# Performance work log

Measured on AMD Instinct MI355X. Metric: run time of the kernel, lower is better.

Reference implementation:

```python
import jax, jax.numpy as jnp
import numpy as np

EMBED_DIM = 1024
NUM_HEADS = 16
HEAD_DIM = EMBED_DIM // NUM_HEADS


def setup_inputs() -> dict:
    key = jax.random.key(0)
    ks = jax.random.split(key, 11)
    B, S, D = 4, 2048, EMBED_DIM
    s = 1.0 / np.sqrt(D)
    return {
        "query": jax.random.normal(ks[0], (B, S, D), jnp.float32),
        "key": jax.random.normal(ks[1], (B, S, D), jnp.float32),
        "value": jax.random.normal(ks[2], (B, S, D), jnp.float32),
        "Wq": jax.random.normal(ks[3], (D, D), jnp.float32) * s,
        "bq": jnp.zeros((D,), jnp.float32),
        "Wk": jax.random.normal(ks[4], (D, D), jnp.float32) * s,
        "bk": jnp.zeros((D,), jnp.float32),
        "Wv": jax.random.normal(ks[5], (D, D), jnp.float32) * s,
        "bv": jnp.zeros((D,), jnp.float32),
        "Wo": jax.random.normal(ks[6], (D, D), jnp.float32) * s,
        "bo": jnp.zeros((D,), jnp.float32),
    }


def _split_heads(x):
    B, S, D = x.shape
    return x.reshape(B, S, NUM_HEADS, HEAD_DIM).transpose(0, 2, 1, 3)  # (B,H,S,hd)


def reference(query, key, value, Wq, bq, Wk, bk, Wv, bv, Wo, bo):
    q = _split_heads(query @ Wq + bq)
    k = _split_heads(key @ Wk + bk)
    v = _split_heads(value @ Wv + bv)
    # naive scaled dot-product attention: full (B,H,S,S) scores materialized
    scores = jnp.einsum("bhqd,bhkd->bhqk", q, k) / np.sqrt(HEAD_DIM).astype(np.float32)
    attn = jax.nn.softmax(scores, axis=-1)
    ctx = jnp.einsum("bhqk,bhkd->bhqd", attn, v)
    B, H, S, hd = ctx.shape
    ctx = ctx.transpose(0, 2, 1, 3).reshape(B, S, H * hd)
    return ctx @ Wo + bo
```

## Files before the change

### kernel.cpp

```cpp
#include <hip/hip_runtime.h>

typedef unsigned short u16;
typedef unsigned int u32;
typedef _Float16 f16;
typedef __attribute__((ext_vector_type(8))) _Float16 f16x8;
typedef __attribute__((ext_vector_type(4))) float f32x4;
typedef __attribute__((ext_vector_type(4))) u32 u32x4;
typedef __attribute__((ext_vector_type(2))) u32 u32x2;
typedef __attribute__((ext_vector_type(4))) u16 u16x4;

static __device__ __forceinline__ u16 f16r(float f) {
  return __builtin_bit_cast(u16, (_Float16)f);
}
static __device__ __forceinline__ u32 packh(float a, float b) {
  return __builtin_bit_cast(u32, __builtin_amdgcn_cvt_pkrtz(a, b));
}
static __device__ __forceinline__ void gload16(const u16* g, u16* l) {
  __builtin_amdgcn_global_load_lds((const __attribute__((address_space(1))) void*)g,
                                   (__attribute__((address_space(3))) void*)l, 16, 0, 0);
}
static __device__ __forceinline__ void gload16f(const float* g, float* l) {
  __builtin_amdgcn_global_load_lds((const __attribute__((address_space(1))) void*)g,
                                   (__attribute__((address_space(3))) void*)l, 16, 0, 0);
}

__global__ __launch_bounds__(256) void wtrans4_k(
    const float* __restrict__ Wq, const float* __restrict__ Wk,
    const float* __restrict__ Wv, const float* __restrict__ Wo,
    u16* __restrict__ Tq, u16* __restrict__ Tk, u16* __restrict__ Tv, u16* __restrict__ To) {
  int z = blockIdx.z;
  const float* W = z == 0 ? Wq : z == 1 ? Wk : z == 2 ? Wv : Wo;
  u16* WT = z == 0 ? Tq : z == 1 ? Tk : z == 2 ? Tv : To;
  __shared__ float tile[32][33];
  int k0 = blockIdx.x * 32, n0 = blockIdx.y * 32;
  int t = threadIdx.x;
  int r = t >> 3, c = (t & 7) * 4;
  f32x4 v = *(const f32x4*)&W[(size_t)(k0 + r) * 1024 + n0 + c];
  tile[r][c + 0] = v[0]; tile[r][c + 1] = v[1]; tile[r][c + 2] = v[2]; tile[r][c + 3] = v[3];
  __syncthreads();
  int n = n0 + (t >> 3), kbase = k0 + (t & 7) * 4;
  u16x4 o;
#pragma unroll
  for (int j = 0; j < 4; j++) o[j] = f16r(tile[(t & 7) * 4 + j][t >> 3]);
  int nt = n >> 7, row = n & 127;
  int kt = kbase >> 5, lc = (kbase >> 3) & 3, e = kbase & 7;
  int pc = lc ^ ((row >> 1) & 3);
  *(u16x4*)&WT[((size_t)(nt * 32 + kt) * 128 + row) * 32 + pc * 8 + e] = o;
}

__global__ __launch_bounds__(256) void gemm_qkv_k(
    const float* __restrict__ Aq, const float* __restrict__ Ak, const float* __restrict__ Av,
    const u16* __restrict__ Tq, const u16* __restrict__ Tk, const u16* __restrict__ Tv,
    const float* __restrict__ bq, const float* __restrict__ bk, const float* __restrict__ bv,
    u16* __restrict__ Qo, u16* __restrict__ Ko, u16* __restrict__ Vo, float qscale) {
  int z = blockIdx.z;
  const float* A = z == 0 ? Aq : z == 1 ? Ak : Av;
  const u16* BT = z == 0 ? Tq : z == 1 ? Tk : Tv;
  const float* bias = z == 0 ? bq : z == 1 ? bk : bv;
  u16* out = z == 0 ? Qo : z == 1 ? Ko : Vo;
  int vmode = (z == 2);
  float scale = z == 0 ? qscale : 1.0f;

  __shared__ float As[2][128 * 32];
  __shared__ u16 Bs[2][128 * 32];
  int lid = blockIdx.x;
  int xcd = lid & 7, idx = lid >> 3;
  int bx = idx & 7, by = xcd * 8 + (idx >> 3);
  int n0 = bx * 128, m0 = by * 128;
  int tid = threadIdx.x, lane = tid & 63;
  int w = tid >> 6, wr = w >> 1, wc = w & 1;
  int fq = lane & 15, fc = lane >> 4;
  f32x4 acc[4][4] = {};
  const u16* BTb = BT + (size_t)bx * 131072;

  auto stage = [&](int ks, int sel) {
    const float* Ab = A + (size_t)m0 * 1024 + ks * 32;
#pragma unroll
    for (int i = 0; i < 4; i++) {
      int u = (w * 4 + i) * 64 + lane;
      int row = u >> 3, pc = u & 7;
      int koff = (pc ^ (row & 7)) << 2;
      gload16f(Ab + (size_t)row * 1024 + koff, &As[sel][(w * 4 + i) * 256]);
    }
    const u16* Bt = BTb + ks * 4096;
#pragma unroll
    for (int i = 0; i < 2; i++)
      gload16(Bt + (w * 2 + i) * 512 + lane * 8, &Bs[sel][(w * 2 + i) * 512]);
  };

  stage(0, 0);
  stage(1, 1);
  for (int ks = 0; ks < 32; ks++) {
    int cur = ks & 1;
    if (ks < 31) asm volatile("s_waitcnt vmcnt(6)" ::: "memory");
    else         asm volatile("s_waitcnt vmcnt(0)" ::: "memory");
    __builtin_amdgcn_s_barrier();
    __builtin_amdgcn_sched_barrier(0);
    f16x8 af[4], bfv[4];
#pragma unroll
    for (int mi = 0; mi < 4; mi++) {
      int row = wr * 64 + mi * 16 + fq;
      int pc0 = (2 * fc) ^ (row & 7);
      f32x4 x0 = *(const f32x4*)&As[cur][row * 32 + pc0 * 4];
      f32x4 x1 = *(const f32x4*)&As[cur][row * 32 + (pc0 ^ 1) * 4];
      u32x4 pk = {packh(x0[0], x0[1]), packh(x0[2], x0[3]),
                  packh(x1[0], x1[1]), packh(x1[2], x1[3])};
      af[mi] = __builtin_bit_cast(f16x8, pk);
    }
#pragma unroll
    for (int ni = 0; ni < 4; ni++) {
      int row = wc * 64 + ni * 16 + fq;
      bfv[ni] = *(const f16x8*)&Bs[cur][row * 32 + (fc ^ ((row >> 1) & 3)) * 8];
    }
    __builtin_amdgcn_s_setprio(1);
#pragma unroll
    for (int mi = 0; mi < 4; mi++)
#pragma unroll
      for (int ni = 0; ni < 4; ni++)
        acc[mi][ni] = __builtin_amdgcn_mfma_f32_16x16x32_f16(af[mi], bfv[ni], acc[mi][ni], 0, 0, 0);
    __builtin_amdgcn_s_setprio(0);
    __builtin_amdgcn_sched_barrier(0);
    __builtin_amdgcn_s_barrier();
    if (ks < 30) stage(ks + 2, cur);
  }
#pragma unroll
  for (int mi = 0; mi < 4; mi++)
#pragma unroll
    for (int ni = 0; ni < 4; ni++) {
      int n = n0 + wc * 64 + ni * 16 + fq;
      float bs = bias[n];
      int h = n >> 6, d = n & 63;
#pragma unroll
      for (int r = 0; r < 4; r++) {
        int m = m0 + wr * 64 + mi * 16 + fc * 4 + r;
        int b = m >> 11, s = m & 2047;
        float v = (acc[mi][ni][r] + bs) * scale;
        size_t o;
        if (vmode == 0) {
          int t = s >> 4, fqo = s & 15, kco = d >> 5, fco = (d & 31) >> 3, e = d & 7;
          o = (size_t)(b * 16 + h) * 131072 + (size_t)((((t * 2 + kco) * 64) + fco * 16 + fqo) * 8 + e);
        } else {
          int kvc = s >> 5, dt = d >> 4, fqo = d & 15, fco = (s & 31) >> 3, e = s & 7;
          o = (size_t)(b * 16 + h) * 131072 + (size_t)((((kvc * 4 + dt) * 64) + fco * 16 + fqo) * 8 + e);
        }
        out[o] = f16r(v);
      }
    }
}

__global__ __launch_bounds__(256) void gemm_o_k(
    const u16* __restrict__ Ag, const u16* __restrict__ Bg,
    const float* __restrict__ bias, float* __restrict__ out) {
  __shared__ u16 SA[2][8192];
  __shared__ u16 SB[2][8192];
  int lid = blockIdx.x;
  int xcd = lid & 7, idx = lid >> 3;
  int bx = idx & 7, by = xcd * 8 + (idx >> 3);
  int n0 = bx * 128, m0 = by * 128;
  int tid = threadIdx.x, lane = tid & 63;
  int w = tid >> 6, wr = w >> 1, wc = w & 1;
  int fq = lane & 15, fc = lane >> 4;
  f32x4 acc[4][4] = {};

  auto stage = [&](int ks, int sel) {
    size_t at = ((size_t)by * 16 + ks) * 8192;
    size_t bt = ((size_t)bx * 32 + ks * 2) * 4096;
#pragma unroll
    for (int i = 0; i < 4; i++) {
      int ub = (w * 4 + i) * 512;
      gload16(Ag + at + ub + lane * 8, &SA[sel][ub]);
      gload16(Bg + bt + ub + lane * 8, &SB[sel][ub]);
    }
  };

  stage(0, 0);
  stage(1, 1);
  for (int ks = 0; ks < 16; ks++) {
    int cur = ks & 1;
    if (ks < 15) asm volatile("s_waitcnt vmcnt(8)" ::: "memory");
    else         asm volatile("s_waitcnt vmcnt(0)" ::: "memory");
    __builtin_amdgcn_s_barrier();
    __builtin_amdgcn_sched_barrier(0);
#pragma unroll
    for (int kc = 0; kc < 2; kc++) {
      f16x8 ah[4], bh[4];
#pragma unroll
      for (int mi = 0; mi < 4; mi++) {
        int row = wr * 64 + mi * 16 + fq;
        ah[mi] = *(const f16x8*)&SA[cur][row * 64 + (((kc * 4 + fc) ^ (row & 7)) << 3)];
      }
#pragma unroll
      for (int ni = 0; ni < 4; ni++) {
        int row = wc * 64 + ni * 16 + fq;
        bh[ni] = *(const f16x8*)&SB[cur][kc * 4096 + row * 32 + (fc ^ ((row >> 1) & 3)) * 8];
      }
      __builtin_amdgcn_s_setprio(1);
#pragma unroll
      for (int mi = 0; mi < 4; mi++)
#pragma unroll
        for (int ni = 0; ni < 4; ni++)
          acc[mi][ni] = __builtin_amdgcn_mfma_f32_16x16x32_f16(ah[mi], bh[ni], acc[mi][ni], 0, 0, 0);
      __builtin_amdgcn_s_setprio(0);
    }
    __builtin_amdgcn_sched_barrier(0);
    __builtin_amdgcn_s_barrier();
    if (ks < 14) stage(ks + 2, cur);
  }
#pragma unroll
  for (int mi = 0; mi < 4; mi++)
#pragma unroll
    for (int ni = 0; ni < 4; ni++) {
      int n = n0 + wc * 64 + ni * 16 + fq;
      float bs = bias[n];
#pragma unroll
      for (int r = 0; r < 4; r++) {
        int m = m0 + wr * 64 + mi * 16 + fc * 4 + r;
        out[(size_t)m * 1024 + n] = acc[mi][ni][r] + bs;
      }
    }
}

__global__ __launch_bounds__(512) void attn_k(
    const u16* __restrict__ Q, const u16* __restrict__ Kg, const u16* __restrict__ Vg,
    u16* __restrict__ ctx) {
  int lid = blockIdx.x;
  int bh = (lid & 7) * 8 + (lid >> 6);
  int qb = (lid >> 3) & 7;
  int tid = threadIdx.x, lane = tid & 63, w = tid >> 6;
  const u16* Qf = Q + (size_t)bh * 131072;
  const u16* Kf = Kg + (size_t)bh * 131072;
  const u16* Vf = Vg + (size_t)bh * 131072;
  int fq = lane & 15, fc = lane >> 4;
  int le = lane * 8;
  int q0 = qb * 256 + w * 32;

  __shared__ u16 KL[2][4096];
  __shared__ u16 VL[2][4096];
  __shared__ u16 P[8][1024];

  f16x8 qf[2][2];
#pragma unroll
  for (int mi = 0; mi < 2; mi++)
#pragma unroll
    for (int kc = 0; kc < 2; kc++)
      qf[mi][kc] = *(const f16x8*)&Qf[((((q0 + 16 * mi) >> 4) * 2 + kc) << 9) + le];

  const f16x8 vones = {(_Float16)1.f, (_Float16)1.f, (_Float16)1.f, (_Float16)1.f,
                       (_Float16)1.f, (_Float16)1.f, (_Float16)1.f, (_Float16)1.f};
  f32x4 O[2][4] = {};
  f32x4 Ol[2] = {};

  int pslot = (fc & 1) * 4;
  int pbase = fq + ((fc >> 1) << 4);

  auto stage = [&](int tt, int bb) {
    int qo = (w & 3) * 1024;
    if (w < 4) {
      const u16* Kt = Kf + tt * 4096;
      gload16(Kt + qo + le, &KL[bb][qo]);
      gload16(Kt + qo + 512 + le, &KL[bb][qo + 512]);
    } else {
      const u16* Vt = Vf + tt * 4096;
      gload16(Vt + qo + le, &VL[bb][qo]);
      gload16(Vt + qo + 512 + le, &VL[bb][qo + 512]);
    }
  };

  stage(0, 0);
  stage(1, 1);
  for (int t = 0; t < 32; t++) {
    int buf = t & 1;
    if (t < 31) asm volatile("s_waitcnt vmcnt(2)" ::: "memory");
    else        asm volatile("s_waitcnt vmcnt(0)" ::: "memory");
    __builtin_amdgcn_s_barrier();
    __builtin_amdgcn_sched_barrier(0);

    f16x8 kf[8];
#pragma unroll
    for (int c = 0; c < 8; c++) kf[c] = *(const f16x8*)&KL[buf][c * 512 + le];

    f32x4 sc[2][4] = {};
    __builtin_amdgcn_s_setprio(1);
#pragma unroll
    for (int mi = 0; mi < 2; mi++)
#pragma unroll
      for (int sub = 0; sub < 4; sub++)
#pragma unroll
        for (int kc = 0; kc < 2; kc++)
          sc[mi][sub] = __builtin_amdgcn_mfma_f32_16x16x32_f16(kf[sub * 2 + kc], qf[mi][kc],
                                                               sc[mi][sub], 0, 0, 0);
    __builtin_amdgcn_s_setprio(0);

    f16x8 vf[8];
#pragma unroll
    for (int c = 0; c < 8; c++) vf[c] = *(const f16x8*)&VL[buf][c * 512 + le];

#pragma unroll
    for (int mi = 0; mi < 2; mi++) {
#pragma unroll
      for (int sub = 0; sub < 4; sub++) {
        float p0 = __builtin_amdgcn_exp2f(sc[mi][sub][0]);
        float p1 = __builtin_amdgcn_exp2f(sc[mi][sub][1]);
        float p2 = __builtin_amdgcn_exp2f(sc[mi][sub][2]);
        float p3 = __builtin_amdgcn_exp2f(sc[mi][sub][3]);
        u32x2 pw = {packh(p0, p1), packh(p2, p3)};
        int lp = (pbase + (sub << 5)) & 63;
        *(u32x2*)&P[w][(sub >> 1) * 512 + lp * 8 + pslot] = pw;
      }
      __builtin_amdgcn_s_setprio(1);
#pragma unroll
      for (int ch = 0; ch < 2; ch++) {
        f16x8 pa = *(const f16x8*)&P[w][ch * 512 + lane * 8];
        Ol[mi] = __builtin_amdgcn_mfma_f32_16x16x32_f16(pa, vones, Ol[mi], 0, 0, 0);
#pragma unroll
        for (int db = 0; db < 4; db++)
          O[mi][db] = __builtin_amdgcn_mfma_f32_16x16x32_f16(pa, vf[ch * 4 + db], O[mi][db], 0, 0, 0);
      }
      __builtin_amdgcn_s_setprio(0);
    }

    __builtin_amdgcn_sched_barrier(0);
    __builtin_amdgcn_s_barrier();
    if (t < 30) stage(t + 2, buf);
  }

  int b = bh >> 4, h = bh & 15;
#pragma unroll
  for (int mi = 0; mi < 2; mi++) {
    float linv[4];
#pragma unroll
    for (int r = 0; r < 4; r++) linv[r] = 1.0f / Ol[mi][r];
#pragma unroll
    for (int db = 0; db < 4; db++)
#pragma unroll
      for (int r = 0; r < 4; r++) {
        float v = O[mi][db][r] * linv[r];
        int s = q0 + mi * 16 + fc * 4 + r;
        int mrow = s & 127, mt = b * 16 + (s >> 7);
        int lc = (db * 16 + fq) >> 3, e = fq & 7;
        int pc = lc ^ (mrow & 7);
        size_t o = ((size_t)(mt * 16 + h) * 128 + mrow) * 64 + pc * 8 + e;
        ctx[o] = f16r(v);
      }
  }
}

extern "C" void kernel_launch(void* const* d_in, const int* in_sizes, int n_in,
                              void* d_out, int out_size, void* d_ws, size_t ws_size,
                              hipStream_t stream) {
  const float* query = (const float*)d_in[0];
  const float* key   = (const float*)d_in[1];
  const float* value = (const float*)d_in[2];
  const float* Wq = (const float*)d_in[3];
  const float* bq = (const float*)d_in[4];
  const float* Wk = (const float*)d_in[5];
  const float* bk = (const float*)d_in[6];
  const float* Wv = (const float*)d_in[7];
  const float* bv = (const float*)d_in[8];
  const float* Wo = (const float*)d_in[9];
  const float* bo = (const float*)d_in[10];
  float* out = (float*)d_out;

  char* ws = (char*)d_ws;
  size_t off = 0;
  auto alloc = [&](size_t bytes) {
    char* p = ws + off;
    off += (bytes + 255) & ~(size_t)255;
    return p;
  };
  u16* WqT = (u16*)alloc(1048576 * 2);
  u16* WkT = (u16*)alloc(1048576 * 2);
  u16* WvT = (u16*)alloc(1048576 * 2);
  u16* WoT = (u16*)alloc(1048576 * 2);
  u16* Qbf = (u16*)alloc((size_t)8388608 * 2);
  u16* Kbf = (u16*)alloc((size_t)8388608 * 2);
  u16* ctx = (u16*)alloc((size_t)8388608 * 2);
  u16* Vfb = (u16*)d_out;

  const float QSCALE = 0.125f * 1.44269504f;

  wtrans4_k<<<dim3(32, 32, 4), 256, 0, stream>>>(Wq, Wk, Wv, Wo, WqT, WkT, WvT, WoT);
  gemm_qkv_k<<<dim3(512, 1, 3), 256, 0, stream>>>(query, key, value, WqT, WkT, WvT,
                                                  bq, bk, bv, Qbf, Kbf, Vfb, QSCALE);
  attn_k<<<512, 512, 0, stream>>>(Qbf, Kbf, Vfb, ctx);
  gemm_o_k<<<512, 256, 0, stream>>>(ctx, WoT, bo, out);
}
```

Baseline: 186.2 us.

## Stage QKV GEMM A tiles through registers and store them to LDS as fp16

The QKV projection GEMM now loads the fp32 activation tile into registers, two stages ahead, and converts it to fp16. It writes the packed values into a swizzled fp16 LDS buffer instead of DMA-ing fp32 straight into LDS and converting after every LDS read. This halves A-tile LDS footprint and read traffic and removes the repeated per-wave conversion on reads. The cost is more VGPRs for the prefetch registers, an extra LDS write with an lgkmcnt wait each step, and vmcnt counting that must now cover the register loads too.

```diff
diff --git a/kernel.cpp b/kernel.cpp
--- a/kernel.cpp
+++ b/kernel.cpp
@@ -16,10 +16,6 @@
   return __builtin_bit_cast(u32, __builtin_amdgcn_cvt_pkrtz(a, b));
 }
 static __device__ __forceinline__ void gload16(const u16* g, u16* l) {
-  __builtin_amdgcn_global_load_lds((const __attribute__((address_space(1))) void*)g,
-                                   (__attribute__((address_space(3))) void*)l, 16, 0, 0);
-}
-static __device__ __forceinline__ void gload16f(const float* g, float* l) {
   __builtin_amdgcn_global_load_lds((const __attribute__((address_space(1))) void*)g,
                                    (__attribute__((address_space(3))) void*)l, 16, 0, 0);
 }
@@ -61,8 +57,8 @@
   int vmode = (z == 2);
   float scale = z == 0 ? qscale : 1.0f;
 
-  __shared__ float As[2][128 * 32];
-  __shared__ u16 Bs[2][128 * 32];
+  __shared__ u16 As[2][4096];
+  __shared__ u16 Bs[2][4096];
   int lid = blockIdx.x;
   int xcd = lid & 7, idx = lid >> 3;
   int bx = idx & 7, by = xcd * 8 + (idx >> 3);
@@ -72,57 +68,73 @@
   int fq = lane & 15, fc = lane >> 4;
   f32x4 acc[4][4] = {};
   const u16* BTb = BT + (size_t)bx * 131072;
-
-  auto stage = [&](int ks, int sel) {
-    const float* Ab = A + (size_t)m0 * 1024 + ks * 32;
-#pragma unroll
-    for (int i = 0; i < 4; i++) {
-      int u = (w * 4 + i) * 64 + lane;
-      int row = u >> 3, pc = u & 7;
-      int koff = (pc ^ (row & 7)) << 2;
-      gload16f(Ab + (size_t)row * 1024 + koff, &As[sel][(w * 4 + i) * 256]);
-    }
-    const u16* Bt = BTb + ks * 4096;
-#pragma unroll
-    for (int i = 0; i < 2; i++)
-      gload16(Bt + (w * 2 + i) * 512 + lane * 8, &Bs[sel][(w * 2 + i) * 512]);
-  };
-
-  stage(0, 0);
-  stage(1, 1);
-  for (int ks = 0; ks < 32; ks++) {
-    int cur = ks & 1;
-    if (ks < 31) asm volatile("s_waitcnt vmcnt(6)" ::: "memory");
-    else         asm volatile("s_waitcnt vmcnt(0)" ::: "memory");
-    __builtin_amdgcn_s_barrier();
-    __builtin_amdgcn_sched_barrier(0);
-    f16x8 af[4], bfv[4];
-#pragma unroll
-    for (int mi = 0; mi < 4; mi++) {
-      int row = wr * 64 + mi * 16 + fq;
-      int pc0 = (2 * fc) ^ (row & 7);
-      f32x4 x0 = *(const f32x4*)&As[cur][row * 32 + pc0 * 4];
-      f32x4 x1 = *(const f32x4*)&As[cur][row * 32 + (pc0 ^ 1) * 4];
-      u32x4 pk = {packh(x0[0], x0[1]), packh(x0[2], x0[3]),
-                  packh(x1[0], x1[1]), packh(x1[2], x1[3])};
-      af[mi] = __builtin_bit_cast(f16x8, pk);
-    }
-#pragma unroll
-    for (int ni = 0; ni < 4; ni++) {
-      int row = wc * 64 + ni * 16 + fq;
-      bfv[ni] = *(const f16x8*)&Bs[cur][row * 32 + (fc ^ ((row >> 1) & 3)) * 8];
-    }
-    __builtin_amdgcn_s_setprio(1);
-#pragma unroll
-    for (int mi = 0; mi < 4; mi++)
-#pragma unroll
-      for (int ni = 0; ni < 4; ni++)
-        acc[mi][ni] = __builtin_amdgcn_mfma_f32_16x16x32_f16(af[mi], bfv[ni], acc[mi][ni], 0, 0, 0);
-    __builtin_amdgcn_s_setprio(0);
-    __builtin_amdgcn_sched_barrier(0);
-    __builtin_amdgcn_s_barrier();
-    if (ks < 30) stage(ks + 2, cur);
-  }
+  const float* Ab = A + (size_t)m0 * 1024;
+
+  int arow0 = tid >> 2;
+  int arow1 = arow0 + 64;
+  int acol = (tid & 3) * 8;
+  int apc = (tid & 3) ^ ((arow0 >> 1) & 3);
+  int aw0 = arow0 * 32 + apc * 8;
+  int aw1 = arow1 * 32 + apc * 8;
+  f32x4 ra[2][4];
+
+#define QKV_LOAD_A(KS, S)                                                       \
+  {                                                                             \
+    const float* Ap = Ab + (KS) * 32 + acol;                                    \
+    ra[S][0] = *(const f32x4*)(Ap + (size_t)arow0 * 1024);                      \
+    ra[S][1] = *(const f32x4*)(Ap + (size_t)arow0 * 1024 + 4);                  \
+    ra[S][2] = *(const f32x4*)(Ap + (size_t)arow1 * 1024);                      \
+    ra[S][3] = *(const f32x4*)(Ap + (size_t)arow1 * 1024 + 4);                  \
+  }
+#define QKV_LOAD_B(KS, S)                                                       \
+  {                                                                             \
+    const u16* Bt = BTb + (KS) * 4096;                                          \
+    gload16(Bt + (w * 2 + 0) * 512 + lane * 8, &Bs[S][(w * 2 + 0) * 512]);      \
+    gload16(Bt + (w * 2 + 1) * 512 + lane * 8, &Bs[S][(w * 2 + 1) * 512]);      \
+  }
+#define QKV_ITER(KS, S)                                                         \
+  {                                                                             \
+    if ((KS) < 31) asm volatile("s_waitcnt vmcnt(6)" ::: "memory");             \
+    else           asm volatile("s_waitcnt vmcnt(0)" ::: "memory");             \
+    u32x4 w0 = {packh(ra[S][0][0], ra[S][0][1]), packh(ra[S][0][2], ra[S][0][3]),\
+                packh(ra[S][1][0], ra[S][1][1]), packh(ra[S][1][2], ra[S][1][3])};\
+    u32x4 w1 = {packh(ra[S][2][0], ra[S][2][1]), packh(ra[S][2][2], ra[S][2][3]),\
+                packh(ra[S][3][0], ra[S][3][1]), packh(ra[S][3][2], ra[S][3][3])};\
+    *(u32x4*)&As[S][aw0] = w0;                                                  \
+    *(u32x4*)&As[S][aw1] = w1;                                                  \
+    asm volatile("s_waitcnt lgkmcnt(0)" ::: "memory");                          \
+    __builtin_amdgcn_s_barrier();                                               \
+    __builtin_amdgcn_sched_barrier(0);                                          \
+    f16x8 af[4], bfv[4];                                                        \
+    _Pragma("unroll") for (int mi = 0; mi < 4; mi++) {                          \
+      int row = wr * 64 + mi * 16 + fq;                                         \
+      af[mi] = *(const f16x8*)&As[S][row * 32 + ((fc ^ ((row >> 1) & 3)) << 3)];\
+    }                                                                           \
+    _Pragma("unroll") for (int ni = 0; ni < 4; ni++) {                          \
+      int row = wc * 64 + ni * 16 + fq;                                         \
+      bfv[ni] = *(const f16x8*)&Bs[S][row * 32 + ((fc ^ ((row >> 1) & 3)) << 3)];\
+    }                                                                           \
+    __builtin_amdgcn_s_setprio(1);                                              \
+    _Pragma("unroll") for (int mi = 0; mi < 4; mi++)                            \
+      _Pragma("unroll") for (int ni = 0; ni < 4; ni++)                          \
+        acc[mi][ni] =                                                           \
+            __builtin_amdgcn_mfma_f32_16x16x32_f16(af[mi], bfv[ni], acc[mi][ni], 0, 0, 0); \
+    __builtin_amdgcn_s_setprio(0);                                              \
+    __builtin_amdgcn_sched_barrier(0);                                          \
+    __builtin_amdgcn_s_barrier();                                               \
+    if ((KS) < 30) { QKV_LOAD_A((KS) + 2, S); QKV_LOAD_B((KS) + 2, S); }        \
+  }
+
+  QKV_LOAD_A(0, 0); QKV_LOAD_B(0, 0);
+  QKV_LOAD_A(1, 1); QKV_LOAD_B(1, 1);
+  for (int kk2 = 0; kk2 < 16; kk2++) {
+    QKV_ITER(kk2 * 2, 0);
+    QKV_ITER(kk2 * 2 + 1, 1);
+  }
+#undef QKV_LOAD_A
+#undef QKV_LOAD_B
+#undef QKV_ITER
+
 #pragma unroll
   for (int mi = 0; mi < 4; mi++)
 #pragma unroll
```

Measured after the change: 184.7 us. About the same (-0.8%).
